# Optimization experiments

Measured on AMD Instinct MI355X. Metric: run time of the kernel, lower is better.

The kernel has to match this reference:

```python
import jax, jax.numpy as jnp
import numpy as np


def _scattering(image, mags, phases):
    # image: [B,S,S] real; mags/phases: [J,L,S,S] real (Fourier-domain Morlet filters)
    J = mags.shape[0]
    psi = (mags * jnp.exp(1j * phases)).astype(jnp.complex64)        # [J,L,S,S]
    xf = jnp.fft.fft2(image)                                          # [B,S,S] complex64
    # first-order: modulus of wavelet convolutions, all scales/orientations at once
    u1 = jnp.abs(jnp.fft.ifft2(xf[:, None, None] * psi[None]))        # [B,J,L,S,S]
    s0 = image.mean(axis=(-2, -1))                                    # [B]
    s1 = u1.mean(axis=(2, 3, 4))                                      # [B,J] (orientation-averaged)
    # second-order: only j2 > j1 (the nan-filtered entries in the original)
    s2_parts = []
    for j1 in range(J - 1):  # structural loop over scales, not data dims
        u1f = jnp.fft.fft2(u1[:, j1].astype(jnp.complex64))           # [B,L1,S,S]
        psi2 = psi[j1 + 1:]                                           # [J2,L2,S,S]
        v = jnp.abs(jnp.fft.ifft2(u1f[:, :, None, None] * psi2[None, None]))  # [B,L1,J2,L2,S,S]
        s2_parts.append(v.mean(axis=(1, 3, 4, 5)))                    # [B,J2]
    s2 = jnp.concatenate(s2_parts, axis=1)                            # [B, J*(J-1)/2]
    return s0, s1, s2


def setup_inputs() -> dict:
    key = jax.random.key(0)
    ks = jax.random.split(key, 8)
    B, S, J, L = 64, 128, 6, 4
    return {
        "image_batch": jax.random.normal(ks[0], (B, S, S), dtype=jnp.float32),
        "mags": jax.random.uniform(ks[1], (J, L, S, S), dtype=jnp.float32),
        "phases": jax.random.normal(ks[2], (J, L, S, S), dtype=jnp.float32),
        "w1": jax.random.normal(ks[3], (22, 16), dtype=jnp.float32) * 0.1,
        "b1": jnp.zeros((16,), dtype=jnp.float32),
        "w2": jax.random.normal(ks[4], (16, 16), dtype=jnp.float32) * 0.1,
        "b2": jnp.zeros((16,), dtype=jnp.float32),
        "w3": jax.random.normal(ks[5], (16, 1), dtype=jnp.float32) * 0.1,
        "b3": jnp.zeros((1,), dtype=jnp.float32),
    }


def reference(image_batch, mags, phases, w1, b1, w2, b2, w3, b3):
    s0, s1, s2 = _scattering(image_batch, mags, phases)
    x = jnp.concatenate([s0[:, None], s1, s2], axis=1)                # [B,22]
    x = jax.nn.relu(x @ w1 + b1)
    x = jax.nn.relu(x @ w2 + b2)
    x = jax.nn.sigmoid(x @ w3 + b3)
    return jnp.squeeze(x, axis=1)                                     # [B]
```

## Files before the change

kernel.cpp:

```cpp
#include <hip/hip_runtime.h>
#include <math.h>


#define SDIM 128
#define PLANE 16384
#define PITCH 129
#define NT 1024
#define TWO_PI 6.28318530717958647692f
#define PSIH_SCALE 16.0f

typedef _Float16 h2 __attribute__((ext_vector_type(2)));

constexpr float W16R[8] = {1.f, 0.9238795325f, 0.7071067812f, 0.3826834324f,
                           0.f, -0.3826834324f, -0.7071067812f, -0.9238795325f};
constexpr float W16I[8] = {0.f, -0.3826834324f, -0.7071067812f, -0.9238795325f,
                           -1.f, -0.9238795325f, -0.7071067812f, -0.3826834324f};

__device__ __forceinline__ float fast_sqrtf(float x) { return __builtin_amdgcn_sqrtf(x); }

__device__ __forceinline__ unsigned packbf(float re, float im) {
  const unsigned r = __float_as_uint(re) + 0x8000u;
  const unsigned i = __float_as_uint(im) + 0x8000u;
  return __builtin_amdgcn_perm(r, i, 0x07060302u);
}
__device__ __forceinline__ void unpackbf(unsigned u, float& re, float& im) {
  re = __uint_as_float(u & 0xFFFF0000u);
  im = __uint_as_float(u << 16);
}

union UHU { unsigned u; h2 h; };
__device__ __forceinline__ h2 u2h(unsigned u) { UHU x; x.u = u; return x.h; }
__device__ __forceinline__ unsigned h2u(h2 h) { UHU x; x.h = h; return x.u; }
__device__ __forceinline__ h2 bch2(float f) { const _Float16 h = (_Float16)f; h2 v = {h, h}; return v; }
__device__ __forceinline__ h2 mkh2(float a, float b) { h2 v = {(_Float16)a, (_Float16)b}; return v; }

__device__ __forceinline__ void stC(float2* s, int idx, float re, float im) { s[idx] = make_float2(re, im); }
__device__ __forceinline__ void ldC(const float2* s, int idx, float& re, float& im) { const float2 v = s[idx]; re = v.x; im = v.y; }
__device__ __forceinline__ void stC(unsigned* s, int idx, float re, float im) { s[idx] = packbf(re, im); }
__device__ __forceinline__ void ldC(const unsigned* s, int idx, float& re, float& im) { unpackbf(s[idx], re, im); }

__device__ __forceinline__ void load_tw(const float2* __restrict__ twg, int g,
                                        float* twr, float* twi) {
#pragma unroll
  for (int k = 1; k < 16; ++k) {
    const float2 w = twg[16 * g + k];
    twr[k] = __uint_as_float(__builtin_amdgcn_readfirstlane(__float_as_uint(w.x)));
    twi[k] = __uint_as_float(__builtin_amdgcn_readfirstlane(__float_as_uint(w.y)));
  }
}
__device__ __forceinline__ void load_twh(const uint2* __restrict__ twgh, int g,
                                         unsigned* twru, unsigned* twiu) {
#pragma unroll
  for (int k = 1; k < 16; ++k) {
    const uint2 w = twgh[16 * g + k];
    twru[k] = (unsigned)__builtin_amdgcn_readfirstlane((int)w.x);
    twiu[k] = (unsigned)__builtin_amdgcn_readfirstlane((int)w.y);
  }
}

template<bool INV>
__device__ __forceinline__ void bfly(float& ar, float& ai, float& br, float& bi, const int idx) {
  float tr, ti;
  if (idx == 0) { tr = br; ti = bi; }
  else if (idx == 4) {
    if (INV) { tr = -bi; ti = br; } else { tr = bi; ti = -br; }
  } else {
    const float wr = W16R[idx];
    const float wi = INV ? -W16I[idx] : W16I[idx];
    tr = br * wr - bi * wi;
    ti = br * wi + bi * wr;
  }
  br = ar - tr; bi = ai - ti;
  ar = ar + tr; ai = ai + ti;
}

#define CSWAP(re, im, a, b) { float _t = re[a]; re[a]=re[b]; re[b]=_t; _t = im[a]; im[a]=im[b]; im[b]=_t; }

template<bool INV>
__device__ __forceinline__ void dft16(float* re, float* im) {
  CSWAP(re, im, 1, 8) CSWAP(re, im, 2, 4) CSWAP(re, im, 3, 12)
  CSWAP(re, im, 5, 10) CSWAP(re, im, 7, 14) CSWAP(re, im, 11, 13)
#pragma unroll
  for (int ls = 1; ls <= 4; ++ls) {
    const int len = 1 << ls, half = len >> 1, tstep = 16 >> ls;
#pragma unroll
    for (int blk = 0; blk < 16; blk += len)
#pragma unroll
      for (int j = 0; j < half; ++j)
        bfly<INV>(re[blk + j], im[blk + j], re[blk + j + half], im[blk + j + half], j * tstep);
  }
}

template<bool INV>
__device__ __forceinline__ void dft8(float* re, float* im) {
  CSWAP(re, im, 1, 4) CSWAP(re, im, 3, 6)
#pragma unroll
  for (int ls = 1; ls <= 3; ++ls) {
    const int len = 1 << ls, half = len >> 1, tstep = 8 >> ls;
#pragma unroll
    for (int blk = 0; blk < 8; blk += len)
#pragma unroll
      for (int j = 0; j < half; ++j)
        bfly<INV>(re[blk + j], im[blk + j], re[blk + j + half], im[blk + j + half], j * tstep * 2);
  }
}

__device__ __forceinline__ void twmul_fwd(float* R, float* I, const float* twr, const float* twi) {
#pragma unroll
  for (int k = 1; k < 16; ++k) {
    const float r = R[k] * twr[k] - I[k] * twi[k];
    I[k] = R[k] * twi[k] + I[k] * twr[k]; R[k] = r;
  }
}
__device__ __forceinline__ void twmul_inv(float* R, float* I, const float* twr, const float* twi) {
#pragma unroll
  for (int k = 1; k < 16; ++k) {
    const float r = R[k] * twr[k] + I[k] * twi[k];
    I[k] = I[k] * twr[k] - R[k] * twi[k]; R[k] = r;
  }
}

template<typename S>
__device__ __forceinline__ void fwd_fft2(float* R, float* I, S* sC,
                                         int g, int q, const float* twr, const float* twi) {
  const int rb = q * PITCH;
  dft16<false>(R, I);
  twmul_fwd(R, I, twr, twi);
  __syncthreads();
#pragma unroll
  for (int k = 0; k < 16; ++k) stC(sC, rb + 8 * k + g, R[k], I[k]);
  __syncthreads();
#pragma unroll
  for (int t = 0; t < 8; ++t) {
    ldC(sC, rb + 16 * g + t, R[t], I[t]);
    ldC(sC, rb + 16 * g + 8 + t, R[8 + t], I[8 + t]);
  }
  dft8<false>(R, I); dft8<false>(R + 8, I + 8);
#pragma unroll
  for (int k2 = 0; k2 < 8; ++k2) {
    stC(sC, rb + 16 * g + k2, R[k2], I[k2]);
    stC(sC, rb + 16 * g + 8 + k2, R[8 + k2], I[8 + k2]);
  }
  __syncthreads();
#pragma unroll
  for (int m = 0; m < 16; ++m) ldC(sC, (g + 8 * m) * PITCH + q, R[m], I[m]);
  dft16<false>(R, I);
  twmul_fwd(R, I, twr, twi);
#pragma unroll
  for (int k = 0; k < 16; ++k) stC(sC, (8 * k + g) * PITCH + q, R[k], I[k]);
  __syncthreads();
#pragma unroll
  for (int u = 0; u < 8; ++u) {
    const int bp = (16 * g + 2 * u) * PITCH + q;
    ldC(sC, bp, R[2 * u], I[2 * u]);
    ldC(sC, bp + PITCH, R[2 * u + 1], I[2 * u + 1]);
  }
  dft8<false>(R, I); dft8<false>(R + 8, I + 8);
}

template<bool FIRST, typename S>
__device__ __forceinline__ void inv_fft2(float* R, float* I, S* sC,
                                         int g, int q, const float* twr, const float* twi) {
  const int rb = q * PITCH;
  dft8<true>(R, I); dft8<true>(R + 8, I + 8);
  if constexpr (!FIRST) __syncthreads();
#pragma unroll
  for (int t = 0; t < 16; ++t) stC(sC, rb + 16 * g + t, R[t], I[t]);
  __syncthreads();
#pragma unroll
  for (int k = 0; k < 16; ++k) ldC(sC, rb + 8 * k + g, R[k], I[k]);
  twmul_inv(R, I, twr, twi);
  dft16<true>(R, I);
#pragma unroll
  for (int m = 0; m < 16; ++m) stC(sC, rb + g + 8 * m, R[m], I[m]);
  __syncthreads();
#pragma unroll
  for (int u = 0; u < 8; ++u) {
    const int bp = (16 * g + 2 * u) * PITCH + q;
    ldC(sC, bp, R[2 * u], I[2 * u]);
    ldC(sC, bp + PITCH, R[2 * u + 1], I[2 * u + 1]);
  }
  dft8<true>(R, I); dft8<true>(R + 8, I + 8);
#pragma unroll
  for (int u = 0; u < 8; ++u) {
    const int bp = (16 * g + 2 * u) * PITCH + q;
    stC(sC, bp, R[2 * u], I[2 * u]);
    stC(sC, bp + PITCH, R[2 * u + 1], I[2 * u + 1]);
  }
  __syncthreads();
#pragma unroll
  for (int k = 0; k < 16; ++k) ldC(sC, (8 * k + g) * PITCH + q, R[k], I[k]);
  twmul_inv(R, I, twr, twi);
  dft16<true>(R, I);
}

__device__ __forceinline__ void bfly_h_inv(h2& ar, h2& ai, h2& br, h2& bi, const int idx) {
  h2 tr, ti;
  if (idx == 0) { tr = br; ti = bi; }
  else if (idx == 4) { tr = -bi; ti = br; }
  else {
    const h2 wr = bch2(W16R[idx]);
    const h2 wi = bch2(-W16I[idx]);
    tr = br * wr - bi * wi;
    ti = br * wi + bi * wr;
  }
  br = ar - tr; bi = ai - ti;
  ar = ar + tr; ai = ai + ti;
}

#define HSWAP(re, im, a, b) { h2 _t = re[a]; re[a]=re[b]; re[b]=_t; _t = im[a]; im[a]=im[b]; im[b]=_t; }

__device__ __forceinline__ void dft16h(h2* re, h2* im) {
  HSWAP(re, im, 1, 8) HSWAP(re, im, 2, 4) HSWAP(re, im, 3, 12)
  HSWAP(re, im, 5, 10) HSWAP(re, im, 7, 14) HSWAP(re, im, 11, 13)
#pragma unroll
  for (int ls = 1; ls <= 4; ++ls) {
    const int len = 1 << ls, half = len >> 1, tstep = 16 >> ls;
#pragma unroll
    for (int blk = 0; blk < 16; blk += len)
#pragma unroll
      for (int j = 0; j < half; ++j)
        bfly_h_inv(re[blk + j], im[blk + j], re[blk + j + half], im[blk + j + half], j * tstep);
  }
}

__device__ __forceinline__ void dft8h(h2* re, h2* im) {
  HSWAP(re, im, 1, 4) HSWAP(re, im, 3, 6)
#pragma unroll
  for (int ls = 1; ls <= 3; ++ls) {
    const int len = 1 << ls, half = len >> 1, tstep = 8 >> ls;
#pragma unroll
    for (int blk = 0; blk < 8; blk += len)
#pragma unroll
      for (int j = 0; j < half; ++j)
        bfly_h_inv(re[blk + j], im[blk + j], re[blk + j + half], im[blk + j + half], j * tstep * 2);
  }
}

__device__ __forceinline__ void twmul_inv_h(h2* R, h2* I, const unsigned* twru, const unsigned* twiu) {
#pragma unroll
  for (int k = 1; k < 16; ++k) {
    const h2 wr = u2h(twru[k]), wi = u2h(twiu[k]);
    const h2 r = R[k] * wr + I[k] * wi;
    I[k] = I[k] * wr - R[k] * wi;
    R[k] = r;
  }
}

__device__ __forceinline__ void inv_rp_core(h2* R2, h2* I2, uint2* sU,
                                            int g, int q,
                                            const unsigned* twru, const unsigned* twiu) {
  const int sb = q * PITCH;
  dft8h(R2, I2); dft8h(R2 + 8, I2 + 8);
#pragma unroll
  for (int s = 0; s < 16; ++s) sU[sb + 16 * g + s] = make_uint2(h2u(R2[s]), h2u(I2[s]));
  __syncthreads();
#pragma unroll
  for (int k = 0; k < 16; ++k) { const uint2 v = sU[sb + 8 * k + g]; R2[k] = u2h(v.x); I2[k] = u2h(v.y); }
  twmul_inv_h(R2, I2, twru, twiu);
  dft16h(R2, I2);
#pragma unroll
  for (int m = 0; m < 16; ++m) sU[sb + g + 8 * m] = make_uint2(h2u(R2[m]), h2u(I2[m]));
  __syncthreads();
  {
    const int s_base = (16 * g) & 63;
    const unsigned sel = (g < 4) ? 0x05040100u : 0x07060302u;
#pragma unroll
    for (int j = 0; j < 16; ++j) {
      const int cb = (s_base + j) * PITCH;
      const uint2 vA = sU[cb + q];
      const uint2 vB = sU[cb + q + 64];
      R2[j] = u2h(__builtin_amdgcn_perm(vB.x, vA.x, sel));
      I2[j] = u2h(__builtin_amdgcn_perm(vB.y, vA.y, sel));
    }
  }
  dft8h(R2, I2); dft8h(R2 + 8, I2 + 8);
  __syncthreads();
#pragma unroll
  for (int s = 0; s < 16; ++s) sU[sb + 16 * g + s] = make_uint2(h2u(R2[s]), h2u(I2[s]));
  __syncthreads();
#pragma unroll
  for (int k = 0; k < 16; ++k) { const uint2 v = sU[sb + 8 * k + g]; R2[k] = u2h(v.x); I2[k] = u2h(v.y); }
  twmul_inv_h(R2, I2, twru, twiu);
  dft16h(R2, I2);
}

template<int NW>
__device__ __forceinline__ float block_reduce_sum(float v, float* red, int tid) {
#pragma unroll
  for (int o = 32; o > 0; o >>= 1) v += __shfl_down(v, o);
  __syncthreads();
  if ((tid & 63) == 0) red[tid >> 6] = v;
  __syncthreads();
  float t = 0.0f;
  if (tid == 0) {
#pragma unroll
    for (int w = 0; w < NW; ++w) t += red[w];
  }
  return t;
}

__global__ __launch_bounds__(256) void k_psi(const float* __restrict__ mags,
                                             const float* __restrict__ phases,
                                             float2* __restrict__ psi,
                                             float2* __restrict__ twg,
                                             uint2* __restrict__ psih,
                                             uint2* __restrict__ twgh) {
  if (blockIdx.x == 0 && threadIdx.x < 128) {
    const int gg = threadIdx.x >> 4, k = threadIdx.x & 15;
    float sn, cs;
    __sincosf(-TWO_PI * (float)(gg * k) * (1.0f / 128.0f), &sn, &cs);
    twg[threadIdx.x] = make_float2(cs, sn);
    twgh[threadIdx.x] = make_uint2(h2u(bch2(cs)), h2u(bch2(sn)));
  }
  const int gid = blockIdx.x * 256 + threadIdx.x;
  if (gid < 24 * PLANE) {
    const int p = gid >> 14;
    const int rem = gid & (PLANE - 1);
    const int e = rem & 1;
    const int tt = (rem >> 1) & 1023;
    const int i = rem >> 11;
    const int j = 2 * i + e;
    const int g = tt >> 7, q = tt & 127;
    const int pr = 16 * g + j, pc = q;
    const int kr = (pr >> 3) + 16 * (pr & 7);
    const int kc = (pc >> 3) + 16 * (pc & 7);
    const int src = (p << 14) + kr * SDIM + kc;
    const float m = mags[src] * (1.0f / 16384.0f);
    float sn, cs;
    __sincosf(phases[src], &sn, &cs);
    psi[gid] = make_float2(m * cs, m * sn);
  } else if (gid < 24 * PLANE + 20 * 8192) {
    const int c = gid - 24 * PLANE;
    const int pidx = c >> 13;
    const int rem = c & 8191;
    const int j = rem >> 9;
    const int t512 = rem & 511;
    const int g = t512 >> 6, q = t512 & 63;
    const int row = 16 * g + j;
    const int plane = pidx + 4;
    const int kr = (row >> 3) + 16 * (row & 7);
    const int kc0 = (q >> 3) + 16 * (q & 7);
    const int q1 = q + 64;
    const int kc1 = (q1 >> 3) + 16 * (q1 & 7);
    const int src0 = (plane << 14) + kr * SDIM + kc0;
    const int src1 = (plane << 14) + kr * SDIM + kc1;
    const float scl = PSIH_SCALE / 16384.0f;
    const float m0 = mags[src0] * scl;
    const float m1 = mags[src1] * scl;
    float sn0, cs0, sn1, cs1;
    __sincosf(phases[src0], &sn0, &cs0);
    __sincosf(phases[src1], &sn1, &cs1);
    psih[c] = make_uint2(h2u(mkh2(m0 * cs0, m1 * cs1)), h2u(mkh2(m0 * sn0, m1 * sn1)));
  }
}

__global__ __launch_bounds__(NT) void k_img_fft(const float* __restrict__ img,
                                                float2* __restrict__ Xf,
                                                float* __restrict__ s0,
                                                const float2* __restrict__ twg) {
  __shared__ float2 sC[SDIM * PITCH];
  __shared__ float red[16];
  const int tid = threadIdx.x, b = blockIdx.x;
  const int g = __builtin_amdgcn_readfirstlane(tid >> 7);
  const int q = tid & 127;
  float twr[16], twi[16];
  load_tw(twg, g, twr, twi);
  const float* ip = img + b * PLANE;
  float sum = 0.0f;
#pragma unroll
  for (int kk = 0; kk < 16; ++kk) {
    const int e = tid + kk * NT;
    const float v = ip[e];
    sC[(e >> 7) * PITCH + (e & 127)] = make_float2(v, 0.0f);
    sum += v;
  }
  const float tot = block_reduce_sum<16>(sum, red, tid);
  if (tid == 0) s0[b] = tot * (1.0f / 16384.0f);
  __syncthreads();
  float R[16], I[16];
#pragma unroll
  for (int m = 0; m < 16; ++m) { R[m] = sC[q * PITCH + g + 8 * m].x; I[m] = 0.0f; }
  fwd_fft2(R, I, sC, g, q, twr, twi);
  float4* x4 = (float4*)Xf + (size_t)b * 8192 + tid;
#pragma unroll
  for (int i = 0; i < 8; ++i)
    x4[i * 1024] = make_float4(R[2 * i], I[2 * i], R[2 * i + 1], I[2 * i + 1]);
}

__global__ __launch_bounds__(NT) void k_scat_a(const float2* __restrict__ Xf,
                                               const float2* __restrict__ psi,
                                               float* __restrict__ s1num,
                                               unsigned* __restrict__ Ubuf,
                                               const float2* __restrict__ twg) {
  __shared__ unsigned sU[SDIM * PITCH];
  __shared__ float red[16];
  const int tid = threadIdx.x;
  const int g = __builtin_amdgcn_readfirstlane(tid >> 7);
  const int q = tid & 127;
  float twr[16], twi[16];
  load_tw(twg, g, twr, twi);
  const int bid = blockIdx.x;
  float R[16], I[16];

  if (bid < 1280) {
    const int j1 = bid >> 8;
    const int b = (bid & 255) >> 2;
    const int l1 = bid & 3;
    const float4* x4 = (const float4*)Xf + (size_t)b * 8192 + tid;
    const float4* p4 = (const float4*)psi + (size_t)(j1 * 4 + l1) * 8192 + tid;
#pragma unroll
    for (int i = 0; i < 8; ++i) {
      const float4 x = x4[i * 1024], v = p4[i * 1024];
      R[2 * i]     = x.x * v.x - x.y * v.y;  I[2 * i]     = x.x * v.y + x.y * v.x;
      R[2 * i + 1] = x.z * v.z - x.w * v.w;  I[2 * i + 1] = x.z * v.w + x.w * v.z;
    }
    inv_fft2<true>(R, I, sU, g, q, twr, twi);
    float s1sum = 0.0f;
#pragma unroll
    for (int m = 0; m < 16; ++m) {
      const float a = fast_sqrtf(R[m] * R[m] + I[m] * I[m]);
      s1sum += a; R[m] = a; I[m] = 0.0f;
    }
    fwd_fft2(R, I, sU, g, q, twr, twi);
    uint4 ob[4];
    unsigned* obs = (unsigned*)ob;
#pragma unroll
    for (int j = 0; j < 16; ++j) obs[j] = packbf(R[j], I[j]);
    uint4* o4 = (uint4*)Ubuf + (size_t)((b * 5 + j1) * 4 + l1) * 4096 + tid;
#pragma unroll
    for (int i = 0; i < 4; ++i) o4[i * 1024] = ob[i];
    const float tot = block_reduce_sum<16>(s1sum, red, tid);
    if (tid == 0) atomicAdd(&s1num[b * 6 + j1], tot);
  } else {
    const int idx = bid - 1280;
    const int b = idx >> 2, l = idx & 3;
    const float4* x4 = (const float4*)Xf + (size_t)b * 8192 + tid;
    const float4* p4 = (const float4*)psi + (size_t)(20 + l) * 8192 + tid;
#pragma unroll
    for (int i = 0; i < 8; ++i) {
      const float4 x = x4[i * 1024], v = p4[i * 1024];
      R[2 * i]     = x.x * v.x - x.y * v.y;  I[2 * i]     = x.x * v.y + x.y * v.x;
      R[2 * i + 1] = x.z * v.z - x.w * v.w;  I[2 * i + 1] = x.z * v.w + x.w * v.z;
    }
    inv_fft2<true>(R, I, sU, g, q, twr, twi);
    float s = 0.0f;
#pragma unroll
    for (int m = 0; m < 16; ++m) s += fast_sqrtf(R[m] * R[m] + I[m] * I[m]);
    const float tot = block_reduce_sum<16>(s, red, tid);
    if (tid == 0) atomicAdd(&s1num[b * 6 + 5], tot);
  }
}

__global__ __launch_bounds__(512, 4) void k_scat_b_rpm(const uint2* __restrict__ psih,
                                                       const unsigned* __restrict__ Ubuf,
                                                       float* __restrict__ s2num,
                                                       const uint2* __restrict__ twgh) {
  __shared__ uint2 sU[64 * PITCH];
  __shared__ float red[8];
  const int tid = threadIdx.x;
  const int g = __builtin_amdgcn_readfirstlane(tid >> 6);
  const int q = tid & 63;
  unsigned twru[16], twiu[16];
  load_twh(twgh, g, twru, twiu);
  const int bid = blockIdx.x;
  const int j1 = bid >> 8;
  const int b = (bid & 255) >> 2;
  const int l1 = bid & 3;
  const int pb = (j1 * (11 - j1)) >> 1;
  const int nit = (5 - j1) * 4;

  h2 UR2[16], UI2[16];
  {
    const uint4* u4 = (const uint4*)Ubuf + (size_t)((b * 5 + j1) * 4 + l1) * 4096;
    const int t0 = g * 128 + q;
    uint4 ua[4], ub[4];
#pragma unroll
    for (int i = 0; i < 4; ++i) { ua[i] = u4[i * 1024 + t0]; ub[i] = u4[i * 1024 + t0 + 64]; }
    const unsigned* uas = (const unsigned*)ua;
    const unsigned* ubs = (const unsigned*)ub;
#pragma unroll
    for (int j = 0; j < 16; ++j) {
      float urL, uiL, urH, uiH;
      unpackbf(uas[j], urL, uiL);
      unpackbf(ubs[j], urH, uiH);
      UR2[j] = mkh2(urL, urH);
      UI2[j] = mkh2(uiL, uiH);
    }
  }

  uint2 buf[16];
  {
    const uint2* ph = psih + (size_t)(4 * j1) * 8192 + tid;
#pragma unroll
    for (int j = 0; j < 16; ++j) buf[j] = ph[j * 512];
  }

  float vsum = 0.0f;
  for (int it = 0; it < nit; ++it) {
    h2 R2[16], I2[16];
#pragma unroll
    for (int j = 0; j < 16; ++j) {
      const h2 pr = u2h(buf[j].x), pi = u2h(buf[j].y);
      R2[j] = UR2[j] * pr - UI2[j] * pi;
      I2[j] = UR2[j] * pi + UI2[j] * pr;
    }
    if (it + 1 < nit) {
      const uint2* phn = psih + (size_t)(4 * j1 + it + 1) * 8192 + tid;
#pragma unroll
      for (int j = 0; j < 16; ++j) buf[j] = phn[j * 512];
    }
    if (it) __syncthreads();
    inv_rp_core(R2, I2, sU, g, q, twru, twiu);
#pragma unroll
    for (int m = 0; m < 16; ++m) {
      const float rl = (float)R2[m].x, il = (float)I2[m].x;
      const float rh = (float)R2[m].y, ih = (float)I2[m].y;
      vsum += fast_sqrtf(rl * rl + il * il) + fast_sqrtf(rh * rh + ih * ih);
    }
    if ((it & 3) == 3) {
      const float tot = block_reduce_sum<8>(vsum, red, tid);
      if (tid == 0) atomicAdd(&s2num[b * 15 + pb + (it >> 2)], tot);
      vsum = 0.0f;
    }
  }
}

__global__ __launch_bounds__(NT) void k_scat_b(const float2* __restrict__ psi,
                                               const unsigned* __restrict__ Ubuf,
                                               float* __restrict__ s2num,
                                               const float2* __restrict__ twg) {
  __shared__ unsigned sU[SDIM * PITCH];
  __shared__ float red[16];
  const int tid = threadIdx.x;
  const int g = __builtin_amdgcn_readfirstlane(tid >> 7);
  const int q = tid & 127;
  float twr[16], twi[16];
  load_tw(twg, g, twr, twi);
  int t = blockIdx.x;
  const int l2 = t & 3; t >>= 2;
  const int pair = t % 15; t /= 15;
  const int l1 = t & 3;
  const int b = t >> 2;
  int j1 = 0, base = 0;
  if (pair >= 14)      { j1 = 4; base = 14; }
  else if (pair >= 12) { j1 = 3; base = 12; }
  else if (pair >= 9)  { j1 = 2; base = 9; }
  else if (pair >= 5)  { j1 = 1; base = 5; }
  const int j2 = j1 + 1 + (pair - base);
  float R[16], I[16];
  {
    const uint4* u4 = (const uint4*)Ubuf + (size_t)((b * 5 + j1) * 4 + l1) * 4096 + tid;
    uint4 ub[4];
#pragma unroll
    for (int i = 0; i < 4; ++i) ub[i] = u4[i * 1024];
    const unsigned* ubs = (const unsigned*)ub;
    const float4* p4 = (const float4*)psi + (size_t)(j2 * 4 + l2) * 8192 + tid;
#pragma unroll
    for (int i = 0; i < 8; ++i) {
      const float4 v = p4[i * 1024];
      float ur, ui;
      unpackbf(ubs[2 * i], ur, ui);
      R[2 * i] = ur * v.x - ui * v.y;      I[2 * i] = ur * v.y + ui * v.x;
      unpackbf(ubs[2 * i + 1], ur, ui);
      R[2 * i + 1] = ur * v.z - ui * v.w;  I[2 * i + 1] = ur * v.w + ui * v.z;
    }
  }
  inv_fft2<true>(R, I, sU, g, q, twr, twi);
  float vsum = 0.0f;
#pragma unroll
  for (int m = 0; m < 16; ++m) vsum += fast_sqrtf(R[m] * R[m] + I[m] * I[m]);
  const float tot = block_reduce_sum<16>(vsum, red, tid);
  if (tid == 0) atomicAdd(&s2num[b * 15 + pair], tot);
}

__global__ __launch_bounds__(NT) void k_scat_mono(const float2* __restrict__ Xf,
                                                  const float2* __restrict__ psi,
                                                  float* __restrict__ s1num,
                                                  float* __restrict__ s2num,
                                                  const float2* __restrict__ twg) {
  __shared__ unsigned sU[SDIM * PITCH];
  __shared__ float red[16];
  const int tid = threadIdx.x;
  const int g = __builtin_amdgcn_readfirstlane(tid >> 7);
  const int q = tid & 127;
  float twr[16], twi[16];
  load_tw(twg, g, twr, twi);
  const int bid = blockIdx.x;
  float R[16], I[16];
  if (bid < 1280) {
    const int j1 = bid >> 8;
    const int b = (bid & 255) >> 2;
    const int l1 = bid & 3;
    const float4* x4 = (const float4*)Xf + (size_t)b * 8192 + tid;
    const float4* p4 = (const float4*)psi + (size_t)(j1 * 4 + l1) * 8192 + tid;
#pragma unroll
    for (int i = 0; i < 8; ++i) {
      const float4 x = x4[i * 1024], v = p4[i * 1024];
      R[2 * i]     = x.x * v.x - x.y * v.y;  I[2 * i]     = x.x * v.y + x.y * v.x;
      R[2 * i + 1] = x.z * v.z - x.w * v.w;  I[2 * i + 1] = x.z * v.w + x.w * v.z;
    }
    inv_fft2<true>(R, I, sU, g, q, twr, twi);
    float s1sum = 0.0f;
#pragma unroll
    for (int m = 0; m < 16; ++m) {
      const float a = fast_sqrtf(R[m] * R[m] + I[m] * I[m]);
      s1sum += a; R[m] = a; I[m] = 0.0f;
    }
    fwd_fft2(R, I, sU, g, q, twr, twi);
    float Ur[16], Ui[16];
#pragma unroll
    for (int k = 0; k < 16; ++k) { Ur[k] = R[k]; Ui[k] = I[k]; }
    {
      const float tot = block_reduce_sum<16>(s1sum, red, tid);
      if (tid == 0) atomicAdd(&s1num[b * 6 + j1], tot);
    }
    const int pb = (j1 * (11 - j1)) >> 1;
    int plane = (j1 + 1) * 4;
#pragma unroll 1
    for (int j2 = j1 + 1; j2 <= 5; ++j2) {
      float vsum = 0.0f;
#pragma unroll 1
      for (int l2 = 0; l2 < 4; ++l2) {
        const float4* q4 = (const float4*)psi + (size_t)plane * 8192 + tid;
#pragma unroll
        for (int i = 0; i < 8; ++i) {
          const float4 v = q4[i * 1024];
          R[2 * i]     = Ur[2 * i] * v.x - Ui[2 * i] * v.y;
          I[2 * i]     = Ur[2 * i] * v.y + Ui[2 * i] * v.x;
          R[2 * i + 1] = Ur[2 * i + 1] * v.z - Ui[2 * i + 1] * v.w;
          I[2 * i + 1] = Ur[2 * i + 1] * v.w + Ui[2 * i + 1] * v.z;
        }
        inv_fft2<false>(R, I, sU, g, q, twr, twi);
#pragma unroll
        for (int m = 0; m < 16; ++m) vsum += fast_sqrtf(R[m] * R[m] + I[m] * I[m]);
        ++plane;
      }
      const float tot = block_reduce_sum<16>(vsum, red, tid);
      if (tid == 0) atomicAdd(&s2num[b * 15 + pb + (j2 - j1 - 1)], tot);
    }
  } else {
    const int idx = bid - 1280;
    const int b = idx >> 2, l = idx & 3;
    const float4* x4 = (const float4*)Xf + (size_t)b * 8192 + tid;
    const float4* p4 = (const float4*)psi + (size_t)(20 + l) * 8192 + tid;
#pragma unroll
    for (int i = 0; i < 8; ++i) {
      const float4 x = x4[i * 1024], v = p4[i * 1024];
      R[2 * i]     = x.x * v.x - x.y * v.y;  I[2 * i]     = x.x * v.y + x.y * v.x;
      R[2 * i + 1] = x.z * v.z - x.w * v.w;  I[2 * i + 1] = x.z * v.w + x.w * v.z;
    }
    inv_fft2<true>(R, I, sU, g, q, twr, twi);
    float s = 0.0f;
#pragma unroll
    for (int m = 0; m < 16; ++m) s += fast_sqrtf(R[m] * R[m] + I[m] * I[m]);
    const float tot = block_reduce_sum<16>(s, red, tid);
    if (tid == 0) atomicAdd(&s1num[b * 6 + 5], tot);
  }
}

__global__ __launch_bounds__(64) void k_final(const float* __restrict__ s0,
                                              const float* __restrict__ s1num,
                                              const float* __restrict__ s2num,
                                              const float* __restrict__ w1,
                                              const float* __restrict__ b1,
                                              const float* __restrict__ w2,
                                              const float* __restrict__ b2,
                                              const float* __restrict__ w3,
                                              const float* __restrict__ b3,
                                              float* __restrict__ out,
                                              float s2scale) {
  const int b = threadIdx.x;
  if (b >= 64) return;
  float x[22];
  x[0] = s0[b];
#pragma unroll
  for (int j = 0; j < 6; ++j) x[1 + j] = s1num[b * 6 + j] * (1.0f / (4.0f * 16384.0f));
#pragma unroll
  for (int p = 0; p < 15; ++p) x[7 + p] = s2num[b * 15 + p] * s2scale;
  float h1[16];
#pragma unroll
  for (int o = 0; o < 16; ++o) {
    float t = b1[o];
    for (int i = 0; i < 22; ++i) t += x[i] * w1[i * 16 + o];
    h1[o] = fmaxf(t, 0.0f);
  }
  float h2a[16];
#pragma unroll
  for (int o = 0; o < 16; ++o) {
    float t = b2[o];
    for (int i = 0; i < 16; ++i) t += h1[i] * w2[i * 16 + o];
    h2a[o] = fmaxf(t, 0.0f);
  }
  float t = b3[0];
#pragma unroll
  for (int i = 0; i < 16; ++i) t += h2a[i] * w3[i];
  out[b] = 1.0f / (1.0f + expf(-t));
}

extern "C" void kernel_launch(void* const* d_in, const int* in_sizes, int n_in,
                              void* d_out, int out_size, void* d_ws, size_t ws_size,
                              hipStream_t stream) {
  (void)in_sizes; (void)n_in; (void)out_size;
  const float* image  = (const float*)d_in[0];
  const float* mags   = (const float*)d_in[1];
  const float* phases = (const float*)d_in[2];
  const float* w1 = (const float*)d_in[3];
  const float* b1 = (const float*)d_in[4];
  const float* w2 = (const float*)d_in[5];
  const float* b2 = (const float*)d_in[6];
  const float* w3 = (const float*)d_in[7];
  const float* b3 = (const float*)d_in[8];
  float* out = (float*)d_out;

  char* ws = (char*)d_ws;
  float2* psi = (float2*)ws;
  float2* Xf  = (float2*)(ws + 3145728);
  float*  s0  = (float*)(ws + 11534336);
  float*  s1n = s0 + 64;
  float*  s2n = s1n + 384;
  float2* twg = (float2*)(s2n + 960);
  uint2*  twgh = (uint2*)((char*)twg + 1024);
  unsigned* Ubuf = (unsigned*)(ws + 11542528);
  uint2*  psih = (uint2*)(ws + 95428608);
  const size_t need_r5 = 11542528ull + 83886080ull;
  const size_t need_h2 = need_r5 + 1310720ull;

  hipMemsetAsync(s1n, 0, (384 + 960) * sizeof(float), stream);
  if (ws_size >= need_h2) {
    k_psi<<<dim3(2176), dim3(256), 0, stream>>>(mags, phases, psi, twg, psih, twgh);
    k_img_fft<<<dim3(64), dim3(NT), 0, stream>>>(image, Xf, s0, twg);
    k_scat_a<<<dim3(1536), dim3(NT), 0, stream>>>(Xf, psi, s1n, Ubuf, twg);
    k_scat_b_rpm<<<dim3(1280), dim3(512), 0, stream>>>(psih, Ubuf, s2n, twgh);
    k_final<<<dim3(1), dim3(64), 0, stream>>>(s0, s1n, s2n, w1, b1, w2, b2, w3, b3, out,
                                              1.0f / (16.0f * 16384.0f * PSIH_SCALE));
  } else if (ws_size >= need_r5) {
    k_psi<<<dim3(1536), dim3(256), 0, stream>>>(mags, phases, psi, twg, psih, twgh);
    k_img_fft<<<dim3(64), dim3(NT), 0, stream>>>(image, Xf, s0, twg);
    k_scat_a<<<dim3(1536), dim3(NT), 0, stream>>>(Xf, psi, s1n, Ubuf, twg);
    k_scat_b<<<dim3(15360), dim3(NT), 0, stream>>>(psi, Ubuf, s2n, twg);
    k_final<<<dim3(1), dim3(64), 0, stream>>>(s0, s1n, s2n, w1, b1, w2, b2, w3, b3, out,
                                              1.0f / (16.0f * 16384.0f));
  } else {
    k_psi<<<dim3(1536), dim3(256), 0, stream>>>(mags, phases, psi, twg, psih, twgh);
    k_img_fft<<<dim3(64), dim3(NT), 0, stream>>>(image, Xf, s0, twg);
    k_scat_mono<<<dim3(1536), dim3(NT), 0, stream>>>(Xf, psi, s1n, s2n, twg);
    k_final<<<dim3(1), dim3(64), 0, stream>>>(s0, s1n, s2n, w1, b1, w2, b2, w3, b3, out,
                                              1.0f / (16.0f * 16384.0f));
  }
}
```

Before: 446.8 us.

## Port first-order scattering stage to packed fp16 half-rate FFT kernel

Replaces the fp32 first-order kernel with a 512-thread variant that does the inverse FFT, modulus and forward FFT of u1 in packed half2 arithmetic. Each thread handles two columns per register, and the input is scaled by a constant to keep fp16 in range. The output is written in a perm-packed fp16 layout that the second-order kernel now reads directly, which removes the bf16 unpack and repack. This halves LDS and register traffic, at the cost of fp16 precision in the first-order modulus and the s1 sums.

```diff
diff --git a/kernel.cpp b/kernel.cpp
--- a/kernel.cpp
+++ b/kernel.cpp
@@ -8,6 +8,7 @@
 #define NT 1024
 #define TWO_PI 6.28318530717958647692f
 #define PSIH_SCALE 16.0f
+#define A_SCALE 16.0f
 
 typedef _Float16 h2 __attribute__((ext_vector_type(2)));
 
@@ -33,6 +34,9 @@
 __device__ __forceinline__ unsigned h2u(h2 h) { UHU x; x.h = h; return x.u; }
 __device__ __forceinline__ h2 bch2(float f) { const _Float16 h = (_Float16)f; h2 v = {h, h}; return v; }
 __device__ __forceinline__ h2 mkh2(float a, float b) { h2 v = {(_Float16)a, (_Float16)b}; return v; }
+
+#define SEL_LO 0x05040100u
+#define SEL_HI 0x07060302u
 
 __device__ __forceinline__ void stC(float2* s, int idx, float re, float im) { s[idx] = make_float2(re, im); }
 __device__ __forceinline__ void ldC(const float2* s, int idx, float& re, float& im) { const float2 v = s[idx]; re = v.x; im = v.y; }
@@ -194,13 +198,15 @@
   dft16<true>(R, I);
 }
 
-__device__ __forceinline__ void bfly_h_inv(h2& ar, h2& ai, h2& br, h2& bi, const int idx) {
+template<bool INV>
+__device__ __forceinline__ void bfly_h(h2& ar, h2& ai, h2& br, h2& bi, const int idx) {
   h2 tr, ti;
   if (idx == 0) { tr = br; ti = bi; }
-  else if (idx == 4) { tr = -bi; ti = br; }
-  else {
+  else if (idx == 4) {
+    if (INV) { tr = -bi; ti = br; } else { tr = bi; ti = -br; }
+  } else {
     const h2 wr = bch2(W16R[idx]);
-    const h2 wi = bch2(-W16I[idx]);
+    const h2 wi = bch2(INV ? -W16I[idx] : W16I[idx]);
     tr = br * wr - bi * wi;
     ti = br * wi + bi * wr;
   }
@@ -210,6 +216,7 @@
 
 #define HSWAP(re, im, a, b) { h2 _t = re[a]; re[a]=re[b]; re[b]=_t; _t = im[a]; im[a]=im[b]; im[b]=_t; }
 
+template<bool INV>
 __device__ __forceinline__ void dft16h(h2* re, h2* im) {
   HSWAP(re, im, 1, 8) HSWAP(re, im, 2, 4) HSWAP(re, im, 3, 12)
   HSWAP(re, im, 5, 10) HSWAP(re, im, 7, 14) HSWAP(re, im, 11, 13)
@@ -220,10 +227,11 @@
     for (int blk = 0; blk < 16; blk += len)
 #pragma unroll
       for (int j = 0; j < half; ++j)
-        bfly_h_inv(re[blk + j], im[blk + j], re[blk + j + half], im[blk + j + half], j * tstep);
-  }
-}
-
+        bfly_h<INV>(re[blk + j], im[blk + j], re[blk + j + half], im[blk + j + half], j * tstep);
+  }
+}
+
+template<bool INV>
 __device__ __forceinline__ void dft8h(h2* re, h2* im) {
   HSWAP(re, im, 1, 4) HSWAP(re, im, 3, 6)
 #pragma unroll
@@ -233,7 +241,7 @@
     for (int blk = 0; blk < 8; blk += len)
 #pragma unroll
       for (int j = 0; j < half; ++j)
-        bfly_h_inv(re[blk + j], im[blk + j], re[blk + j + half], im[blk + j + half], j * tstep * 2);
+        bfly_h<INV>(re[blk + j], im[blk + j], re[blk + j + half], im[blk + j + half], j * tstep * 2);
   }
 }
 
@@ -246,25 +254,34 @@
     R[k] = r;
   }
 }
+__device__ __forceinline__ void twmul_fwd_h(h2* R, h2* I, const unsigned* twru, const unsigned* twiu) {
+#pragma unroll
+  for (int k = 1; k < 16; ++k) {
+    const h2 wr = u2h(twru[k]), wi = u2h(twiu[k]);
+    const h2 r = R[k] * wr - I[k] * wi;
+    I[k] = R[k] * wi + I[k] * wr;
+    R[k] = r;
+  }
+}
 
 __device__ __forceinline__ void inv_rp_core(h2* R2, h2* I2, uint2* sU,
                                             int g, int q,
                                             const unsigned* twru, const unsigned* twiu) {
   const int sb = q * PITCH;
-  dft8h(R2, I2); dft8h(R2 + 8, I2 + 8);
+  dft8h<true>(R2, I2); dft8h<true>(R2 + 8, I2 + 8);
 #pragma unroll
   for (int s = 0; s < 16; ++s) sU[sb + 16 * g + s] = make_uint2(h2u(R2[s]), h2u(I2[s]));
   __syncthreads();
 #pragma unroll
   for (int k = 0; k < 16; ++k) { const uint2 v = sU[sb + 8 * k + g]; R2[k] = u2h(v.x); I2[k] = u2h(v.y); }
   twmul_inv_h(R2, I2, twru, twiu);
-  dft16h(R2, I2);
+  dft16h<true>(R2, I2);
 #pragma unroll
   for (int m = 0; m < 16; ++m) sU[sb + g + 8 * m] = make_uint2(h2u(R2[m]), h2u(I2[m]));
   __syncthreads();
   {
     const int s_base = (16 * g) & 63;
-    const unsigned sel = (g < 4) ? 0x05040100u : 0x07060302u;
+    const unsigned sel = (g < 4) ? SEL_LO : SEL_HI;
 #pragma unroll
     for (int j = 0; j < 16; ++j) {
       const int cb = (s_base + j) * PITCH;
@@ -274,7 +291,7 @@
       I2[j] = u2h(__builtin_amdgcn_perm(vB.y, vA.y, sel));
     }
   }
-  dft8h(R2, I2); dft8h(R2 + 8, I2 + 8);
+  dft8h<true>(R2, I2); dft8h<true>(R2 + 8, I2 + 8);
   __syncthreads();
 #pragma unroll
   for (int s = 0; s < 16; ++s) sU[sb + 16 * g + s] = make_uint2(h2u(R2[s]), h2u(I2[s]));
@@ -282,7 +299,45 @@
 #pragma unroll
   for (int k = 0; k < 16; ++k) { const uint2 v = sU[sb + 8 * k + g]; R2[k] = u2h(v.x); I2[k] = u2h(v.y); }
   twmul_inv_h(R2, I2, twru, twiu);
-  dft16h(R2, I2);
+  dft16h<true>(R2, I2);
+}
+
+__device__ __forceinline__ void fwd_rp_core(h2* R2, h2* I2, uint2* sU,
+                                            int g, int q,
+                                            const unsigned* twru, const unsigned* twiu) {
+  const int sb = q * PITCH;
+  dft16h<false>(R2, I2);
+  twmul_fwd_h(R2, I2, twru, twiu);
+#pragma unroll
+  for (int k = 0; k < 16; ++k) sU[sb + 8 * k + g] = make_uint2(h2u(R2[k]), h2u(I2[k]));
+  __syncthreads();
+#pragma unroll
+  for (int t = 0; t < 16; ++t) { const uint2 v = sU[sb + 16 * g + t]; R2[t] = u2h(v.x); I2[t] = u2h(v.y); }
+  dft8h<false>(R2, I2); dft8h<false>(R2 + 8, I2 + 8);
+#pragma unroll
+  for (int t = 0; t < 16; ++t) sU[sb + 16 * g + t] = make_uint2(h2u(R2[t]), h2u(I2[t]));
+  __syncthreads();
+  {
+#pragma unroll
+    for (int u = 0; u < 8; ++u) {
+      const int cb = (g + 8 * u) * PITCH;
+      const uint2 vA = sU[cb + q];
+      const uint2 vB = sU[cb + q + 64];
+      R2[u]     = u2h(__builtin_amdgcn_perm(vB.x, vA.x, SEL_LO));
+      I2[u]     = u2h(__builtin_amdgcn_perm(vB.y, vA.y, SEL_LO));
+      R2[u + 8] = u2h(__builtin_amdgcn_perm(vB.x, vA.x, SEL_HI));
+      I2[u + 8] = u2h(__builtin_amdgcn_perm(vB.y, vA.y, SEL_HI));
+    }
+  }
+  dft16h<false>(R2, I2);
+  twmul_fwd_h(R2, I2, twru, twiu);
+  __syncthreads();
+#pragma unroll
+  for (int k = 0; k < 16; ++k) sU[sb + 8 * k + g] = make_uint2(h2u(R2[k]), h2u(I2[k]));
+  __syncthreads();
+#pragma unroll
+  for (int t = 0; t < 16; ++t) { const uint2 v = sU[sb + 16 * g + t]; R2[t] = u2h(v.x); I2[t] = u2h(v.y); }
+  dft8h<false>(R2, I2); dft8h<false>(R2 + 8, I2 + 8);
 }
 
 template<int NW>
@@ -388,6 +443,91 @@
     x4[i * 1024] = make_float4(R[2 * i], I[2 * i], R[2 * i + 1], I[2 * i + 1]);
 }
 
+__global__ __launch_bounds__(512, 4) void k_scat_a_rp(const float2* __restrict__ Xf,
+                                                      const float2* __restrict__ psi,
+                                                      float* __restrict__ s1num,
+                                                      unsigned* __restrict__ Ubuf,
+                                                      const uint2* __restrict__ twgh) {
+  __shared__ uint2 sU[64 * PITCH];
+  __shared__ float red[8];
+  const int tid = threadIdx.x;
+  const int g = __builtin_amdgcn_readfirstlane(tid >> 6);
+  const int q = tid & 63;
+  unsigned twru[16], twiu[16];
+  load_twh(twgh, g, twru, twiu);
+  const int bid = blockIdx.x;
+
+  int plane, b, sidx, grp = -1;
+  if (bid < 1280) {
+    const int j1 = bid >> 8;
+    b = (bid & 255) >> 2;
+    const int l1 = bid & 3;
+    plane = j1 * 4 + l1;
+    sidx = b * 6 + j1;
+    grp = (b * 5 + j1) * 4 + l1;
+  } else {
+    const int idx = bid - 1280;
+    b = idx >> 2;
+    plane = 20 + (idx & 3);
+    sidx = b * 6 + 5;
+  }
+
+  h2 R2[16], I2[16];
+  {
+    const int t0 = g * 128 + q;
+    const float4* xL = (const float4*)Xf + (size_t)b * 8192 + t0;
+    const float4* pL = (const float4*)psi + (size_t)plane * 8192 + t0;
+#pragma unroll
+    for (int i = 0; i < 8; ++i) {
+      const float4 xa = xL[i * 1024],      va = pL[i * 1024];
+      const float4 xb = xL[i * 1024 + 64], vb = pL[i * 1024 + 64];
+      const float reL0 = xa.x * va.x - xa.y * va.y, imL0 = xa.x * va.y + xa.y * va.x;
+      const float reH0 = xb.x * vb.x - xb.y * vb.y, imH0 = xb.x * vb.y + xb.y * vb.x;
+      const float reL1 = xa.z * va.z - xa.w * va.w, imL1 = xa.z * va.w + xa.w * va.z;
+      const float reH1 = xb.z * vb.z - xb.w * vb.w, imH1 = xb.z * vb.w + xb.w * vb.z;
+      R2[2 * i]     = mkh2(reL0 * A_SCALE, reH0 * A_SCALE);
+      I2[2 * i]     = mkh2(imL0 * A_SCALE, imH0 * A_SCALE);
+      R2[2 * i + 1] = mkh2(reL1 * A_SCALE, reH1 * A_SCALE);
+      I2[2 * i + 1] = mkh2(imL1 * A_SCALE, imH1 * A_SCALE);
+    }
+  }
+  inv_rp_core(R2, I2, sU, g, q, twru, twiu);
+
+  float s1sum = 0.0f;
+  if (grp >= 0) {
+#pragma unroll
+    for (int m = 0; m < 16; ++m) {
+      const float rl = (float)R2[m].x, il = (float)I2[m].x;
+      const float rh = (float)R2[m].y, ih = (float)I2[m].y;
+      const float aL = fast_sqrtf(rl * rl + il * il);
+      const float aH = fast_sqrtf(rh * rh + ih * ih);
+      s1sum += aL + aH;
+      R2[m] = mkh2(aL * (1.0f / A_SCALE), aH * (1.0f / A_SCALE));
+      I2[m] = bch2(0.0f);
+    }
+    fwd_rp_core(R2, I2, sU, g, q, twru, twiu);
+    uint4* o4 = (uint4*)Ubuf + (size_t)grp * 4096 + tid;
+#pragma unroll
+    for (int i = 0; i < 8; ++i) {
+      uint4 ob;
+      ob.x = __builtin_amdgcn_perm(h2u(I2[2 * i]),     h2u(R2[2 * i]),     SEL_LO);
+      ob.y = __builtin_amdgcn_perm(h2u(I2[2 * i]),     h2u(R2[2 * i]),     SEL_HI);
+      ob.z = __builtin_amdgcn_perm(h2u(I2[2 * i + 1]), h2u(R2[2 * i + 1]), SEL_LO);
+      ob.w = __builtin_amdgcn_perm(h2u(I2[2 * i + 1]), h2u(R2[2 * i + 1]), SEL_HI);
+      o4[i * 512] = ob;
+    }
+  } else {
+#pragma unroll
+    for (int m = 0; m < 16; ++m) {
+      const float rl = (float)R2[m].x, il = (float)I2[m].x;
+      const float rh = (float)R2[m].y, ih = (float)I2[m].y;
+      s1sum += fast_sqrtf(rl * rl + il * il) + fast_sqrtf(rh * rh + ih * ih);
+    }
+  }
+  const float tot = block_reduce_sum<8>(s1sum, red, tid);
+  if (tid == 0) atomicAdd(&s1num[sidx], tot);
+}
+
 __global__ __launch_bounds__(NT) void k_scat_a(const float2* __restrict__ Xf,
                                                const float2* __restrict__ psi,
                                                float* __restrict__ s1num,
@@ -472,20 +612,14 @@
 
   h2 UR2[16], UI2[16];
   {
-    const uint4* u4 = (const uint4*)Ubuf + (size_t)((b * 5 + j1) * 4 + l1) * 4096;
-    const int t0 = g * 128 + q;
-    uint4 ua[4], ub[4];
-#pragma unroll
-    for (int i = 0; i < 4; ++i) { ua[i] = u4[i * 1024 + t0]; ub[i] = u4[i * 1024 + t0 + 64]; }
-    const unsigned* uas = (const unsigned*)ua;
-    const unsigned* ubs = (const unsigned*)ub;
-#pragma unroll
-    for (int j = 0; j < 16; ++j) {
-      float urL, uiL, urH, uiH;
-      unpackbf(uas[j], urL, uiL);
-      unpackbf(ubs[j], urH, uiH);
-      UR2[j] = mkh2(urL, urH);
-      UI2[j] = mkh2(uiL, uiH);
+    const uint4* u4 = (const uint4*)Ubuf + (size_t)((b * 5 + j1) * 4 + l1) * 4096 + tid;
+#pragma unroll
+    for (int i = 0; i < 8; ++i) {
+      const uint4 v = u4[i * 512];
+      UR2[2 * i]     = u2h(__builtin_amdgcn_perm(v.y, v.x, SEL_LO));
+      UI2[2 * i]     = u2h(__builtin_amdgcn_perm(v.y, v.x, SEL_HI));
+      UR2[2 * i + 1] = u2h(__builtin_amdgcn_perm(v.w, v.z, SEL_LO));
+      UI2[2 * i + 1] = u2h(__builtin_amdgcn_perm(v.w, v.z, SEL_HI));
     }
   }
 
@@ -669,13 +803,13 @@
                                               const float* __restrict__ w3,
                                               const float* __restrict__ b3,
                                               float* __restrict__ out,
-                                              float s2scale) {
+                                              float s1scale, float s2scale) {
   const int b = threadIdx.x;
   if (b >= 64) return;
   float x[22];
   x[0] = s0[b];
 #pragma unroll
-  for (int j = 0; j < 6; ++j) x[1 + j] = s1num[b * 6 + j] * (1.0f / (4.0f * 16384.0f));
+  for (int j = 0; j < 6; ++j) x[1 + j] = s1num[b * 6 + j] * s1scale;
 #pragma unroll
   for (int p = 0; p < 15; ++p) x[7 + p] = s2num[b * 15 + p] * s2scale;
   float h1[16];
@@ -730,9 +864,10 @@
   if (ws_size >= need_h2) {
     k_psi<<<dim3(2176), dim3(256), 0, stream>>>(mags, phases, psi, twg, psih, twgh);
     k_img_fft<<<dim3(64), dim3(NT), 0, stream>>>(image, Xf, s0, twg);
-    k_scat_a<<<dim3(1536), dim3(NT), 0, stream>>>(Xf, psi, s1n, Ubuf, twg);
+    k_scat_a_rp<<<dim3(1536), dim3(512), 0, stream>>>(Xf, psi, s1n, Ubuf, twgh);
     k_scat_b_rpm<<<dim3(1280), dim3(512), 0, stream>>>(psih, Ubuf, s2n, twgh);
     k_final<<<dim3(1), dim3(64), 0, stream>>>(s0, s1n, s2n, w1, b1, w2, b2, w3, b3, out,
+                                              1.0f / (4.0f * 16384.0f * A_SCALE),
                                               1.0f / (16.0f * 16384.0f * PSIH_SCALE));
   } else if (ws_size >= need_r5) {
     k_psi<<<dim3(1536), dim3(256), 0, stream>>>(mags, phases, psi, twg, psih, twgh);
@@ -740,12 +875,14 @@
     k_scat_a<<<dim3(1536), dim3(NT), 0, stream>>>(Xf, psi, s1n, Ubuf, twg);
     k_scat_b<<<dim3(15360), dim3(NT), 0, stream>>>(psi, Ubuf, s2n, twg);
     k_final<<<dim3(1), dim3(64), 0, stream>>>(s0, s1n, s2n, w1, b1, w2, b2, w3, b3, out,
+                                              1.0f / (4.0f * 16384.0f),
                                               1.0f / (16.0f * 16384.0f));
   } else {
     k_psi<<<dim3(1536), dim3(256), 0, stream>>>(mags, phases, psi, twg, psih, twgh);
     k_img_fft<<<dim3(64), dim3(NT), 0, stream>>>(image, Xf, s0, twg);
     k_scat_mono<<<dim3(1536), dim3(NT), 0, stream>>>(Xf, psi, s1n, s2n, twg);
     k_final<<<dim3(1), dim3(64), 0, stream>>>(s0, s1n, s2n, w1, b1, w2, b2, w3, b3, out,
+                                              1.0f / (4.0f * 16384.0f),
                                               1.0f / (16.0f * 16384.0f));
   }
 }
```

After: 440.7 us. Within noise of the previous version (-1.4%).
